# Kernel optimization log

Measured on AMD Instinct MI355X. Metric: run time of the kernel, lower is better.

Reference implementation:

```python
import jax, jax.numpy as jnp
import numpy as np

N = 50000
E = 400000
F_IN = 5
H = 8
C1, C2, C3 = 64, 32, 16
NEG_SLOPE = 0.2


def setup_inputs() -> dict:
    key = jax.random.key(0)
    ks = jax.random.split(key, 16)
    s = 0.1  # small init scale
    return {
        "x": jax.random.normal(ks[0], (N, F_IN), jnp.float32),
        "edge_index": jax.random.randint(ks[1], (2, E), 0, N, jnp.int64),
        "edge_weight": jax.random.uniform(ks[2], (E,), jnp.float32),
        "W1": jax.random.normal(ks[3], (F_IN, H * C1), jnp.float32) * s,
        "a_src1": jax.random.normal(ks[4], (H, C1), jnp.float32) * s,
        "a_dst1": jax.random.normal(ks[5], (H, C1), jnp.float32) * s,
        "b1": jnp.zeros((H * C1,), jnp.float32),
        "W2": jax.random.normal(ks[6], (H * C1, H * C2), jnp.float32) * s,
        "a_src2": jax.random.normal(ks[7], (H, C2), jnp.float32) * s,
        "a_dst2": jax.random.normal(ks[8], (H, C2), jnp.float32) * s,
        "b2": jnp.zeros((H * C2,), jnp.float32),
        "Wg": jax.random.normal(ks[9], (H * C2, C3), jnp.float32) * s,
        "bg": jnp.zeros((C3,), jnp.float32),
        "Wfc": jax.random.normal(ks[10], (C3, 1), jnp.float32) * s,
        "bfc": jnp.zeros((1,), jnp.float32),
    }


def _gat_layer(x, W, a_src, a_dst, b, src, dst, n, heads, ch):
    # PyG GATConv (concat=True), eval mode (dropout off), self-loops already in src/dst.
    h = (x @ W).reshape(n, heads, ch)                      # (N, H, C)
    e_s = jnp.sum(h * a_src, axis=-1)                      # (N, H)
    e_d = jnp.sum(h * a_dst, axis=-1)                      # (N, H)
    e = jax.nn.leaky_relu(e_s[src] + e_d[dst], NEG_SLOPE)  # (Etot, H)
    m = jax.ops.segment_max(e, dst, num_segments=n)
    m = jnp.where(jnp.isfinite(m), m, 0.0)                 # guard empty segments
    ex = jnp.exp(e - m[dst])
    den = jax.ops.segment_sum(ex, dst, num_segments=n)
    alpha = ex / (den[dst] + 1e-16)                        # softmax over in-edges
    out = jax.ops.segment_sum(h[src] * alpha[..., None], dst, num_segments=n)
    return out.reshape(n, heads * ch) + b


def _gcn_layer(x, W, b, src, dst, w_full, n):
    # PyG GCNConv with gcn_norm: D^{-1/2} A_hat D^{-1/2}, self-loop weight 1.
    deg = jax.ops.segment_sum(w_full, dst, num_segments=n)
    dinv = jnp.where(deg > 0, jax.lax.rsqrt(deg), 0.0)
    norm = dinv[src] * w_full * dinv[dst]                  # (Etot,)
    h = x @ W                                              # (N, C3)
    out = jax.ops.segment_sum(h[src] * norm[:, None], dst, num_segments=n)
    return out + b


def reference(x, edge_index, edge_weight, W1, a_src1, a_dst1, b1,
              W2, a_src2, a_dst2, b2, Wg, bg, Wfc, bfc):
    n = x.shape[0]
    loops = jnp.arange(n, dtype=edge_index.dtype)
    src = jnp.concatenate([edge_index[0], loops])
    dst = jnp.concatenate([edge_index[1], loops])
    w_full = jnp.concatenate([edge_weight, jnp.ones((n,), edge_weight.dtype)])

    h = _gat_layer(x, W1, a_src1, a_dst1, b1, src, dst, n, H, C1)
    h = jax.nn.elu(h)
    h = _gat_layer(h, W2, a_src2, a_dst2, b2, src, dst, n, H, C2)
    h = jax.nn.elu(h)
    h = _gcn_layer(h, Wg, bg, src, dst, w_full, n)
    h = jax.nn.elu(h)
    out = jax.nn.sigmoid(h @ Wfc + bfc)                    # (N, 1)
    return out
```

## Files before the change

### kernel.cpp

```cpp
#include <hip/hip_runtime.h>
#include <hip/hip_bf16.h>
#include <float.h>
#include <math.h>

#define N_NODES 50000
#define N_EDGES 400000
#define ETOT    (N_EDGES + N_NODES)
#define F_IN    5
#define HEADS   8
#define C1      64
#define C2      32
#define C3      16
#define HC1     (HEADS * C1)
#define HC2     (HEADS * C2)
#define NEG_SLOPE 0.2f
#define NCHUNK  ((N_NODES + 255) / 256)
#define NH8     (N_NODES * HEADS)
#define MPAD    (((N_NODES + 63) / 64) * 64)
#define GCOLS   (HC2 + 16)

typedef short bf16x8 __attribute__((ext_vector_type(8)));
typedef float f32x4  __attribute__((ext_vector_type(4)));
typedef unsigned short ushort_t;
typedef unsigned short ushort8_t __attribute__((ext_vector_type(8)));

__device__ __forceinline__ float eluf(float x) {
    return x > 0.f ? x : (expf(x) - 1.f);
}
__device__ __forceinline__ float bf2f(unsigned short u) {
    union { unsigned int i; float f; } v; v.i = ((unsigned int)u) << 16; return v.f;
}
__device__ __forceinline__ unsigned short f2bf(float f) {
    __hip_bfloat16 b = __float2bfloat16(f);
    return *(unsigned short*)&b;
}
__device__ __forceinline__ float softnum(float es, float ed) {
    float v = es + ed;
    v = v > 0.f ? v : NEG_SLOPE * v;
    return expf(v);
}

__global__ void k_deg(const int* __restrict__ ei, const float* __restrict__ ew,
                      int* degi, float* degf) {
    int i = blockIdx.x * blockDim.x + threadIdx.x;
    if (i >= ETOT) return;
    int d   = (i < N_EDGES) ? ei[N_EDGES + i] : (i - N_EDGES);
    float w = (i < N_EDGES) ? ew[i] : 1.f;
    atomicAdd(&degi[d], 1);
    atomicAdd(&degf[d], w);
}

__global__ void k_scan_a(const int* __restrict__ deg, int* __restrict__ part) {
    __shared__ int lds[256];
    int t = threadIdx.x;
    int i = blockIdx.x * 256 + t;
    lds[t] = (i < N_NODES) ? deg[i] : 0;
    __syncthreads();
    for (int off = 128; off >= 1; off >>= 1) {
        if (t < off) lds[t] += lds[t + off];
        __syncthreads();
    }
    if (t == 0) part[blockIdx.x] = lds[0];
}

__global__ void k_scan_b(int* part) {
    __shared__ int lds[256];
    int t = threadIdx.x;
    int v = (t < NCHUNK) ? part[t] : 0;
    lds[t] = v;
    __syncthreads();
    for (int off = 1; off < 256; off <<= 1) {
        int x = (t >= off) ? lds[t - off] : 0;
        __syncthreads();
        lds[t] += x;
        __syncthreads();
    }
    if (t < NCHUNK) part[t] = lds[t] - v;
}

__global__ void k_scan_c(const int* __restrict__ deg, const int* __restrict__ part,
                         int* __restrict__ offs) {
    __shared__ int lds[256];
    int t = threadIdx.x;
    int i = blockIdx.x * 256 + t;
    int v = (i < N_NODES) ? deg[i] : 0;
    lds[t] = v;
    __syncthreads();
    for (int off = 1; off < 256; off <<= 1) {
        int x = (t >= off) ? lds[t - off] : 0;
        __syncthreads();
        lds[t] += x;
        __syncthreads();
    }
    int excl = part[blockIdx.x] + lds[t] - v;
    if (i < N_NODES) offs[i] = excl;
    if (i == N_NODES - 1) offs[N_NODES] = excl + v;
}

__global__ void k_scatter(const int* __restrict__ ei, const int* __restrict__ offs,
                          int* cursor, int2* __restrict__ csr) {
    int i = blockIdx.x * blockDim.x + threadIdx.x;
    if (i >= ETOT) return;
    int s, d;
    if (i < N_EDGES) { s = ei[i]; d = ei[N_EDGES + i]; }
    else             { s = d = i - N_EDGES; }
    int pos = offs[d] + atomicAdd(&cursor[d], 1);
    csr[pos] = make_int2(s, i);
}

__global__ void k_fold(const float* __restrict__ W1,
                       const float* __restrict__ a_src1, const float* __restrict__ a_dst1,
                       float* __restrict__ as1f, float* __restrict__ ad1f) {
    int idx = threadIdx.x;
    if (idx >= HEADS * F_IN) return;
    int h = idx / F_IN, f = idx % F_IN;
    float s = 0.f, d = 0.f;
    for (int c = 0; c < C1; c++) {
        float w = W1[f * HC1 + h * C1 + c];
        s += w * a_src1[h * C1 + c];
        d += w * a_dst1[h * C1 + c];
    }
    as1f[idx] = s;
    ad1f[idx] = d;
}

__global__ void k_es1(const float* __restrict__ x,
                      const float* __restrict__ as1f, const float* __restrict__ ad1f,
                      float* __restrict__ es, float* __restrict__ ed) {
    int g = blockIdx.x * blockDim.x + threadIdx.x;
    if (g >= NH8) return;
    int n = g >> 3, h = g & 7;
    float vs = 0.f, vd = 0.f;
#pragma unroll
    for (int f = 0; f < F_IN; f++) {
        float xv = x[n * F_IN + f];
        vs += xv * as1f[h * F_IN + f];
        vd += xv * ad1f[h * F_IN + f];
    }
    es[g] = vs;
    ed[g] = vd;
}

__global__ void k_agg_x(const float* __restrict__ x,
                        const float* __restrict__ es1, const float* __restrict__ ed1,
                        const int* __restrict__ offs, const int2* __restrict__ csr,
                        float* __restrict__ aggx) {
    int g = blockIdx.x * blockDim.x + threadIdx.x;
    if (g >= NH8) return;
    int d = g >> 3, h = g & 7;
    float edv = ed1[g];
    int k0 = offs[d], k1 = offs[d + 1];
    float a0 = 0.f, a1 = 0.f, a2 = 0.f, a3 = 0.f, a4 = 0.f, exsum = 0.f;
    for (int k = k0; k < k1; k++) {
        int2 se = csr[k];
        float ex = softnum(es1[se.x * HEADS + h], edv);
        const float* xp = x + se.x * F_IN;
        a0 += ex * xp[0];
        a1 += ex * xp[1];
        a2 += ex * xp[2];
        a3 += ex * xp[3];
        a4 += ex * xp[4];
        exsum += ex;
    }
    float inv = 1.f / (exsum + 1e-16f);
    aggx[0 * NH8 + g] = a0 * inv;
    aggx[1 * NH8 + g] = a1 * inv;
    aggx[2 * NH8 + g] = a2 * inv;
    aggx[3 * NH8 + g] = a3 * inv;
    aggx[4 * NH8 + g] = a4 * inv;
}

__global__ __launch_bounds__(256) void k_expand(const float* __restrict__ aggx,
                                                const float* __restrict__ W1,
                                                const float* __restrict__ b1,
                                                ushort_t* __restrict__ x2bf) {
    int wave = threadIdx.x >> 6;
    int j    = threadIdx.x & 63;
    int n    = blockIdx.x * 4 + wave;
    if (n >= N_NODES) return;
    int h = j >> 3;
    int g = n * HEADS + h;
    float av[F_IN];
#pragma unroll
    for (int f = 0; f < F_IN; f++) av[f] = aggx[f * NH8 + g];

    const float* w1p = W1 + j * 8;
    float4 s0 = *(const float4*)(b1 + j * 8);
    float4 s1 = *(const float4*)(b1 + j * 8 + 4);
#pragma unroll
    for (int f = 0; f < F_IN; f++) {
        float4 w0  = *(const float4*)(w1p + f * HC1);
        float4 w1v = *(const float4*)(w1p + f * HC1 + 4);
        s0.x += av[f] * w0.x;  s0.y += av[f] * w0.y;
        s0.z += av[f] * w0.z;  s0.w += av[f] * w0.w;
        s1.x += av[f] * w1v.x; s1.y += av[f] * w1v.y;
        s1.z += av[f] * w1v.z; s1.w += av[f] * w1v.w;
    }
    ushort8_t o;
    o[0] = f2bf(eluf(s0.x)); o[1] = f2bf(eluf(s0.y));
    o[2] = f2bf(eluf(s0.z)); o[3] = f2bf(eluf(s0.w));
    o[4] = f2bf(eluf(s1.x)); o[5] = f2bf(eluf(s1.y));
    o[6] = f2bf(eluf(s1.z)); o[7] = f2bf(eluf(s1.w));
    *(ushort8_t*)(x2bf + (size_t)n * HC1 + j * 8) = o;
}

__global__ void k_packW2X(const float* __restrict__ W2,
                          const float* __restrict__ a_src2, const float* __restrict__ a_dst2,
                          ushort_t* __restrict__ W2X) {
    int idx = blockIdx.x * blockDim.x + threadIdx.x;
    if (idx >= GCOLS * HC1) return;
    int c = idx >> 9;
    int k = idx & 511;
    float v;
    if (c < HC2) {
        v = W2[(size_t)k * HC2 + c];
    } else {
        int h = (c - HC2) & 7;
        const float* av = (c < HC2 + 8) ? a_src2 : a_dst2;
        v = 0.f;
#pragma unroll 8
        for (int j = 0; j < C2; j++)
            v += W2[(size_t)k * HC2 + h * C2 + j] * av[h * C2 + j];
    }
    W2X[idx] = f2bf(v);
}

__global__ __launch_bounds__(256, 3) void k_gemm_mfma(const short* __restrict__ A,
                                                      const short* __restrict__ W2X,
                                                      ushort_t* __restrict__ h2bf,
                                                      float* __restrict__ es2,
                                                      float* __restrict__ ed2) {
    __shared__ short Bs[GCOLS * 32];
    int t    = threadIdx.x;
    int wave = t >> 6;
    int lane = t & 63;
    int lo   = lane & 15;
    int quad = lane >> 4;
    int m0   = blockIdx.x * 64 + wave * 16;
    const short* ap = A + (size_t)(m0 + lo) * HC1 + quad * 8;

    f32x4 acc[17];
#pragma unroll
    for (int f = 0; f < 17; f++) acc[f] = (f32x4){0.f, 0.f, 0.f, 0.f};

    for (int idx = t; idx < GCOLS * 4; idx += 256) {
        int c = idx >> 2, q = idx & 3;
        int s = (q + c + (c >> 2)) & 3;
        *(bf16x8*)(Bs + c * 32 + s * 8) = *(const bf16x8*)(W2X + (size_t)c * HC1 + q * 8);
    }
    __syncthreads();

#pragma unroll 1
    for (int k0 = 0; k0 < HC1; k0 += 32) {
        int nk = k0 + 32;
        bf16x8 pre[5];
        if (nk < HC1) {
#pragma unroll
            for (int j = 0; j < 5; j++) {
                int idx = t + j * 256;
                if (idx < GCOLS * 4) {
                    int c = idx >> 2, q = idx & 3;
                    pre[j] = *(const bf16x8*)(W2X + (size_t)c * HC1 + nk + q * 8);
                }
            }
        }
        bf16x8 aF = *(const bf16x8*)(ap + k0);
#pragma unroll
        for (int f = 0; f < 17; f++) {
            int c = f * 16 + lo;
            int s = (quad + c + (c >> 2)) & 3;
            bf16x8 bF = *(const bf16x8*)(Bs + c * 32 + s * 8);
            acc[f] = __builtin_amdgcn_mfma_f32_16x16x32_bf16(aF, bF, acc[f], 0, 0, 0);
        }
        __syncthreads();
        if (nk < HC1) {
#pragma unroll
            for (int j = 0; j < 5; j++) {
                int idx = t + j * 256;
                if (idx < GCOLS * 4) {
                    int c = idx >> 2, q = idx & 3;
                    int s = (q + c + (c >> 2)) & 3;
                    *(bf16x8*)(Bs + c * 32 + s * 8) = pre[j];
                }
            }
            __syncthreads();
        }
    }

    int rowb = m0 + quad * 4;
#pragma unroll
    for (int f = 0; f < 16; f++) {
#pragma unroll
        for (int r = 0; r < 4; r++) {
            int row = rowb + r;
            if (row < N_NODES)
                h2bf[(size_t)row * HC2 + f * 16 + lo] = f2bf(acc[f][r]);
        }
    }
#pragma unroll
    for (int r = 0; r < 4; r++) {
        int row = rowb + r;
        if (row < N_NODES) {
            if (lo < 8) es2[row * HEADS + lo]       = acc[16][r];
            else        ed2[row * HEADS + (lo - 8)] = acc[16][r];
        }
    }
}

__global__ __launch_bounds__(256) void k_gat_agg2(const ushort_t* __restrict__ h2bf,
                                                  const float* __restrict__ es2,
                                                  const float* __restrict__ ed2,
                                                  const int* __restrict__ offs,
                                                  const int2* __restrict__ csr,
                                                  const float* __restrict__ b2,
                                                  ushort_t* __restrict__ x3bf) {
    int wave = threadIdx.x >> 6;
    int lane = threadIdx.x & 63;
    int d = blockIdx.x * 4 + wave;
    if (d >= N_NODES) return;
    int c4 = lane * 4;
    int h  = lane >> 3;
    float edv = ed2[d * HEADS + h];
    int k0 = offs[d], k1 = offs[d + 1];
    float acc0 = 0.f, acc1 = 0.f, acc2 = 0.f, acc3 = 0.f, exsum = 0.f;
    int k = k0;
    for (; k + 1 < k1; k += 2) {
        int2 e0 = csr[k];
        int2 e1 = csr[k + 1];
        float x0 = softnum(es2[e0.x * HEADS + h], edv);
        float x1 = softnum(es2[e1.x * HEADS + h], edv);
        ushort4 v0 = *(const ushort4*)(h2bf + (size_t)e0.x * HC2 + c4);
        ushort4 v1 = *(const ushort4*)(h2bf + (size_t)e1.x * HC2 + c4);
        acc0 += x0 * bf2f(v0.x) + x1 * bf2f(v1.x);
        acc1 += x0 * bf2f(v0.y) + x1 * bf2f(v1.y);
        acc2 += x0 * bf2f(v0.z) + x1 * bf2f(v1.z);
        acc3 += x0 * bf2f(v0.w) + x1 * bf2f(v1.w);
        exsum += x0 + x1;
    }
    if (k < k1) {
        int2 e0 = csr[k];
        float x0 = softnum(es2[e0.x * HEADS + h], edv);
        ushort4 v0 = *(const ushort4*)(h2bf + (size_t)e0.x * HC2 + c4);
        acc0 += x0 * bf2f(v0.x);
        acc1 += x0 * bf2f(v0.y);
        acc2 += x0 * bf2f(v0.z);
        acc3 += x0 * bf2f(v0.w);
        exsum += x0;
    }
    float inv = 1.f / (exsum + 1e-16f);
    float4 bias = *(const float4*)(b2 + c4);
    ushort4 o;
    o.x = f2bf(eluf(acc0 * inv + bias.x));
    o.y = f2bf(eluf(acc1 * inv + bias.y));
    o.z = f2bf(eluf(acc2 * inv + bias.z));
    o.w = f2bf(eluf(acc3 * inv + bias.w));
    *(ushort4*)(x3bf + (size_t)d * HC2 + c4) = o;
}

__global__ __launch_bounds__(256) void k_hg(const ushort_t* __restrict__ x3bf,
                                            const float* __restrict__ Wg,
                                            float* __restrict__ hg) {
    __shared__ float xs[16 * HC2];
    int n0 = blockIdx.x * 16;
    int t  = threadIdx.x;
    for (int q = t; q < 16 * HC2 / 4; q += 256) {
        int r  = q >> 6;
        int cc = (q & 63) * 4;
        int n  = n0 + r;
        ushort4 v = make_ushort4(0, 0, 0, 0);
        if (n < N_NODES) v = *(const ushort4*)(x3bf + (size_t)n * HC2 + cc);
        xs[r * HC2 + cc + 0] = bf2f(v.x);
        xs[r * HC2 + cc + 1] = bf2f(v.y);
        xs[r * HC2 + cc + 2] = bf2f(v.z);
        xs[r * HC2 + cc + 3] = bf2f(v.w);
    }
    __syncthreads();
    int r = t >> 4, c = t & 15;
    float acc = 0.f;
#pragma unroll 4
    for (int k = 0; k < HC2; k++) acc += xs[r * HC2 + k] * Wg[k * C3 + c];
    int n = n0 + r;
    if (n < N_NODES) hg[(size_t)n * C3 + c] = acc;
}

__global__ __launch_bounds__(256) void k_gcn_out(const float* __restrict__ hg,
                                                 const float* __restrict__ ew,
                                                 const float* __restrict__ degf,
                                                 const int* __restrict__ offs,
                                                 const int2* __restrict__ csr,
                                                 const float* __restrict__ bg,
                                                 const float* __restrict__ Wfc,
                                                 const float* __restrict__ bfc,
                                                 float* __restrict__ out) {
    int t = threadIdx.x;
    int r = t >> 4, c = t & 15;
    int d = blockIdx.x * 16 + r;
    float val = 0.f;
    if (d < N_NODES) {
        float dd = degf[d];
        float dinv_d = dd > 0.f ? rsqrtf(dd) : 0.f;
        int k0 = offs[d], k1 = offs[d + 1];
        float acc = 0.f;
        for (int k = k0; k < k1; k++) {
            int2 se = csr[k];
            float w = (se.y < N_EDGES) ? ew[se.y] : 1.f;
            float ds_ = degf[se.x];
            float dinv_s = ds_ > 0.f ? rsqrtf(ds_) : 0.f;
            acc += hg[(size_t)se.x * C3 + c] * (dinv_s * w * dinv_d);
        }
        val = eluf(acc + bg[c]);
    }
    float z = val * Wfc[c];
#pragma unroll
    for (int off = 8; off >= 1; off >>= 1) z += __shfl_xor(z, off, 16);
    if (c == 0 && d < N_NODES) out[d] = 1.f / (1.f + expf(-(z + bfc[0])));
}

extern "C" void kernel_launch(void* const* d_in, const int* in_sizes, int n_in,
                              void* d_out, int out_size, void* d_ws, size_t ws_size,
                              hipStream_t stream) {
    const float* x       = (const float*)d_in[0];
    const int*   ei      = (const int*)  d_in[1];
    const float* ew      = (const float*)d_in[2];
    const float* W1      = (const float*)d_in[3];
    const float* a_src1  = (const float*)d_in[4];
    const float* a_dst1  = (const float*)d_in[5];
    const float* b1      = (const float*)d_in[6];
    const float* W2      = (const float*)d_in[7];
    const float* a_src2  = (const float*)d_in[8];
    const float* a_dst2  = (const float*)d_in[9];
    const float* b2      = (const float*)d_in[10];
    const float* Wg      = (const float*)d_in[11];
    const float* bg      = (const float*)d_in[12];
    const float* Wfc     = (const float*)d_in[13];
    const float* bfc     = (const float*)d_in[14];
    float* out = (float*)d_out;

    char* w = (char*)d_ws;
    size_t off = 0;
    auto alloc = [&](size_t bytes) -> void* {
        void* p = w + off;
        off = (off + bytes + 255) & ~(size_t)255;
        return p;
    };
    ushort_t* x2bf = (ushort_t*)alloc((size_t)MPAD * HC1 * 2);
    ushort_t* W2X  = (ushort_t*)alloc((size_t)GCOLS * HC1 * 2);
    ushort_t* h2bf = (ushort_t*)alloc((size_t)N_NODES * HC2 * 2);
    ushort_t* x3bf = (ushort_t*)alloc((size_t)N_NODES * HC2 * 2);
    float* hg     = (float*)alloc((size_t)N_NODES * C3 * 4);
    float* aggx   = (float*)alloc((size_t)F_IN * NH8 * 4);
    float* es1    = (float*)alloc((size_t)NH8 * 4);
    float* ed1    = (float*)alloc((size_t)NH8 * 4);
    float* es2    = (float*)alloc((size_t)NH8 * 4);
    float* ed2    = (float*)alloc((size_t)NH8 * 4);
    float* as1f   = (float*)alloc((size_t)HEADS * F_IN * 4);
    float* ad1f   = (float*)alloc((size_t)HEADS * F_IN * 4);
    float* degf   = (float*)alloc((size_t)N_NODES * 4);
    int*   degi   = (int*)  alloc((size_t)N_NODES * 4);
    int*   cursor = (int*)  alloc((size_t)N_NODES * 4);
    char*  zero_end = w + off;
    int*   offs   = (int*)  alloc((size_t)(N_NODES + 1) * 4);
    int*   part   = (int*)  alloc(256 * 4);
    int2*  csr    = (int2*) alloc((size_t)ETOT * 8);

    const int T = 256;
    hipMemsetAsync(degf, 0, (size_t)(zero_end - (char*)degf), stream);
    k_deg<<<dim3((ETOT + T - 1) / T), dim3(T), 0, stream>>>(ei, ew, degi, degf);
    k_scan_a<<<dim3(NCHUNK), dim3(256), 0, stream>>>(degi, part);
    k_scan_b<<<dim3(1), dim3(256), 0, stream>>>(part);
    k_scan_c<<<dim3(NCHUNK), dim3(256), 0, stream>>>(degi, part, offs);
    k_scatter<<<dim3((ETOT + T - 1) / T), dim3(T), 0, stream>>>(ei, offs, cursor, csr);
    k_fold<<<dim3(1), dim3(128), 0, stream>>>(W1, a_src1, a_dst1, as1f, ad1f);
    k_packW2X<<<dim3((GCOLS * HC1 + T - 1) / T), dim3(T), 0, stream>>>(W2, a_src2, a_dst2, W2X);

    k_es1<<<dim3((NH8 + T - 1) / T), dim3(T), 0, stream>>>(x, as1f, ad1f, es1, ed1);
    k_agg_x<<<dim3((NH8 + T - 1) / T), dim3(T), 0, stream>>>(x, es1, ed1, offs, csr, aggx);
    k_expand<<<dim3((N_NODES + 3) / 4), dim3(256), 0, stream>>>(aggx, W1, b1, x2bf);

    k_gemm_mfma<<<dim3(MPAD / 64), dim3(256), 0, stream>>>(
        (const short*)x2bf, (const short*)W2X, h2bf, es2, ed2);
    k_gat_agg2<<<dim3((N_NODES + 3) / 4), dim3(256), 0, stream>>>(
        h2bf, es2, ed2, offs, csr, b2, x3bf);

    k_hg<<<dim3((N_NODES + 15) / 16), dim3(256), 0, stream>>>(x3bf, Wg, hg);
    k_gcn_out<<<dim3((N_NODES + 15) / 16), dim3(256), 0, stream>>>(
        hg, ew, degf, offs, csr, bg, Wfc, bfc, out);
}
```

Baseline: 339.9 us.

## Give each GEMM wave two row tiles to reuse B fragments

The MFMA GEMM now runs with 3 waves per block and 96 rows per block instead of 4 waves and 64 rows. Each wave computes two 16-row tiles that share every B fragment loaded from LDS. This halves LDS B reads per MFMA and cuts the number of blocks that restage W2X. In exchange each wave holds twice the accumulator registers, and occupancy per CU drops. A buffer allocated at the old MPAD size could be overrun if x2bf padding depends on MPAD.

```diff
diff --git a/kernel.cpp b/kernel.cpp
--- a/kernel.cpp
+++ b/kernel.cpp
@@ -16,7 +16,9 @@
 #define NEG_SLOPE 0.2f
 #define NCHUNK  ((N_NODES + 255) / 256)
 #define NH8     (N_NODES * HEADS)
-#define MPAD    (((N_NODES + 63) / 64) * 64)
+#define MROWS   96
+#define NBLK    ((N_NODES + MROWS - 1) / MROWS)
+#define MPAD    (NBLK * MROWS)
 #define GCOLS   (HC2 + 16)
 
 typedef short bf16x8 __attribute__((ext_vector_type(8)));
@@ -225,7 +227,7 @@
     W2X[idx] = f2bf(v);
 }
 
-__global__ __launch_bounds__(256, 3) void k_gemm_mfma(const short* __restrict__ A,
+__global__ __launch_bounds__(192, 2) void k_gemm_mfma(const short* __restrict__ A,
                                                       const short* __restrict__ W2X,
                                                       ushort_t* __restrict__ h2bf,
                                                       float* __restrict__ es2,
@@ -236,14 +238,16 @@
     int lane = t & 63;
     int lo   = lane & 15;
     int quad = lane >> 4;
-    int m0   = blockIdx.x * 64 + wave * 16;
+    int m0   = blockIdx.x * MROWS + wave * 32;
     const short* ap = A + (size_t)(m0 + lo) * HC1 + quad * 8;
 
-    f32x4 acc[17];
-#pragma unroll
-    for (int f = 0; f < 17; f++) acc[f] = (f32x4){0.f, 0.f, 0.f, 0.f};
-
-    for (int idx = t; idx < GCOLS * 4; idx += 256) {
+    f32x4 acc[2][17];
+#pragma unroll
+    for (int rt = 0; rt < 2; rt++)
+#pragma unroll
+        for (int f = 0; f < 17; f++) acc[rt][f] = (f32x4){0.f, 0.f, 0.f, 0.f};
+
+    for (int idx = t; idx < GCOLS * 4; idx += 192) {
         int c = idx >> 2, q = idx & 3;
         int s = (q + c + (c >> 2)) & 3;
         *(bf16x8*)(Bs + c * 32 + s * 8) = *(const bf16x8*)(W2X + (size_t)c * HC1 + q * 8);
@@ -253,30 +257,32 @@
 #pragma unroll 1
     for (int k0 = 0; k0 < HC1; k0 += 32) {
         int nk = k0 + 32;
-        bf16x8 pre[5];
+        bf16x8 pre[6];
         if (nk < HC1) {
 #pragma unroll
-            for (int j = 0; j < 5; j++) {
-                int idx = t + j * 256;
+            for (int j = 0; j < 6; j++) {
+                int idx = t + j * 192;
                 if (idx < GCOLS * 4) {
                     int c = idx >> 2, q = idx & 3;
                     pre[j] = *(const bf16x8*)(W2X + (size_t)c * HC1 + nk + q * 8);
                 }
             }
         }
-        bf16x8 aF = *(const bf16x8*)(ap + k0);
+        bf16x8 aF0 = *(const bf16x8*)(ap + k0);
+        bf16x8 aF1 = *(const bf16x8*)(ap + (size_t)16 * HC1 + k0);
 #pragma unroll
         for (int f = 0; f < 17; f++) {
             int c = f * 16 + lo;
             int s = (quad + c + (c >> 2)) & 3;
             bf16x8 bF = *(const bf16x8*)(Bs + c * 32 + s * 8);
-            acc[f] = __builtin_amdgcn_mfma_f32_16x16x32_bf16(aF, bF, acc[f], 0, 0, 0);
+            acc[0][f] = __builtin_amdgcn_mfma_f32_16x16x32_bf16(aF0, bF, acc[0][f], 0, 0, 0);
+            acc[1][f] = __builtin_amdgcn_mfma_f32_16x16x32_bf16(aF1, bF, acc[1][f], 0, 0, 0);
         }
         __syncthreads();
         if (nk < HC1) {
 #pragma unroll
-            for (int j = 0; j < 5; j++) {
-                int idx = t + j * 256;
+            for (int j = 0; j < 6; j++) {
+                int idx = t + j * 192;
                 if (idx < GCOLS * 4) {
                     int c = idx >> 2, q = idx & 3;
                     int s = (q + c + (c >> 2)) & 3;
@@ -287,22 +293,25 @@
         }
     }
 
-    int rowb = m0 + quad * 4;
-#pragma unroll
-    for (int f = 0; f < 16; f++) {
+#pragma unroll
+    for (int rt = 0; rt < 2; rt++) {
+        int rowb = m0 + rt * 16 + quad * 4;
+#pragma unroll
+        for (int f = 0; f < 16; f++) {
+#pragma unroll
+            for (int r = 0; r < 4; r++) {
+                int row = rowb + r;
+                if (row < N_NODES)
+                    h2bf[(size_t)row * HC2 + f * 16 + lo] = f2bf(acc[rt][f][r]);
+            }
+        }
 #pragma unroll
         for (int r = 0; r < 4; r++) {
             int row = rowb + r;
-            if (row < N_NODES)
-                h2bf[(size_t)row * HC2 + f * 16 + lo] = f2bf(acc[f][r]);
-        }
-    }
-#pragma unroll
-    for (int r = 0; r < 4; r++) {
-        int row = rowb + r;
-        if (row < N_NODES) {
-            if (lo < 8) es2[row * HEADS + lo]       = acc[16][r];
-            else        ed2[row * HEADS + (lo - 8)] = acc[16][r];
+            if (row < N_NODES) {
+                if (lo < 8) es2[row * HEADS + lo]       = acc[rt][16][r];
+                else        ed2[row * HEADS + (lo - 8)] = acc[rt][16][r];
+            }
         }
     }
 }
@@ -477,7 +486,7 @@
     k_agg_x<<<dim3((NH8 + T - 1) / T), dim3(T), 0, stream>>>(x, es1, ed1, offs, csr, aggx);
     k_expand<<<dim3((N_NODES + 3) / 4), dim3(256), 0, stream>>>(aggx, W1, b1, x2bf);
 
-    k_gemm_mfma<<<dim3(MPAD / 64), dim3(256), 0, stream>>>(
+    k_gemm_mfma<<<dim3(NBLK), dim3(192), 0, stream>>>(
         (const short*)x2bf, (const short*)W2X, h2bf, es2, ed2);
     k_gat_agg2<<<dim3((N_NODES + 3) / 4), dim3(256), 0, stream>>>(
         h2bf, es2, ed2, offs, csr, b2, x3bf);
```

Measured after the change: 359.5 us. 5.8% more time.
